# Optimization experiments

Hardware: AMD Instinct MI355X
Metric: run time of the kernel (lower is better)

## Reference

```python
import jax, jax.numpy as jnp
import numpy as np

B, H, W, L, R = 8, 32, 32, 6, 384
NH = 6                      # num_heads
NE = L * R                  # n_embd = 2304
HID = 4 * NE                # tree-MLP hidden
M = sum(4 ** i for i in range(L))  # 1365 unique tree nodes
EPS = 1e-5


def build_node_id_map(h, w, l):
    # (h,w,level) -> unique node id; level k patches are 2^k x 2^k blocks
    ids = np.zeros((h, w, l), np.int32)
    off = 0
    for k in range(l):
        ws = w >> k
        hh = (np.arange(h) >> k)[:, None]
        ww = (np.arange(w) >> k)[None, :]
        ids[:, :, k] = off + hh * ws + ww
        off += (h >> k) * ws
    assert off == M
    return ids

_IDS = jnp.asarray(build_node_id_map(H, W, L).reshape(-1))  # (H*W*L,)


def layernorm(x, w, b):
    mu = jnp.mean(x, axis=-1, keepdims=True)
    var = jnp.mean(jnp.square(x - mu), axis=-1, keepdims=True)
    return (x - mu) * jax.lax.rsqrt(var + EPS) * w + b


def setup_inputs() -> dict:
    key = jax.random.key(0)
    ks = jax.random.split(key, 12)
    s = 0.02
    return {
        "x": jax.random.normal(ks[0], (B, H, W, L, R), jnp.float32),
        "ln1_w": jnp.ones((R,), jnp.float32), "ln1_b": jnp.zeros((R,), jnp.float32),
        "ln2_w": jnp.ones((R,), jnp.float32), "ln2_b": jnp.zeros((R,), jnp.float32),
        "wq": s * jax.random.normal(ks[1], (R, R), jnp.float32), "bq": jnp.zeros((R,), jnp.float32),
        "wk": s * jax.random.normal(ks[2], (R, R), jnp.float32), "bk": jnp.zeros((R,), jnp.float32),
        "wv": s * jax.random.normal(ks[3], (R, R), jnp.float32), "bv": jnp.zeros((R,), jnp.float32),
        "wo": s * jax.random.normal(ks[4], (R, R), jnp.float32), "bo": jnp.zeros((R,), jnp.float32),
        "w1": s * jax.random.normal(ks[5], (NE, HID), jnp.float32), "b1": jnp.zeros((HID,), jnp.float32),
        "w2": s * jax.random.normal(ks[6], (HID, NE), jnp.float32), "b2": jnp.zeros((NE,), jnp.float32),
    }


def reference(x, ln1_w, ln1_b, ln2_w, ln2_b, wq, bq, wk, bk, wv, bv, wo, bo, w1, b1, w2, b2):
    dh = R // NH
    # (1) LN per node
    x_ln = layernorm(x, ln1_w, ln1_b)
    # (2) unify duplicates -> (B, M, R) via segment mean over node ids
    xf = x_ln.reshape(B, H * W * L, R)
    counts = jnp.zeros((M,), x.dtype).at[_IDS].add(1.0)
    uniq = jnp.zeros((B, M, R), x.dtype).at[:, _IDS].add(xf) / counts[None, :, None]
    # (3) multi-head self-attention over the M unique tree nodes
    q = (uniq @ wq + bq).reshape(B, M, NH, dh)
    k = (uniq @ wk + bk).reshape(B, M, NH, dh)
    v = (uniq @ wv + bv).reshape(B, M, NH, dh)
    logits = jnp.einsum("bmhd,bnhd->bhmn", q, k) * (1.0 / jnp.sqrt(jnp.asarray(dh, x.dtype)))
    attn = jax.nn.softmax(logits, axis=-1)
    o = jnp.einsum("bhmn,bnhd->bmhd", attn, v).reshape(B, M, R)
    attn_out = o @ wo + bo
    # (4) scatter back to (B,H,W,L,R)
    x_attn = attn_out[:, _IDS].reshape(B, H, W, L, R)
    # (5) residual (dropout is identity in eval)
    x_res = x + x_attn
    # (6) LN -> tree MLP over full level stack at each (h,w)
    x_ln2 = layernorm(x_res, ln2_w, ln2_b)
    flat = x_ln2.reshape(B, H, W, NE)
    h1 = jax.nn.gelu(flat @ w1 + b1)
    mlp_out = (h1 @ w2 + b2).reshape(B, H, W, L, R)
    # (7) residual
    return x_res + mlp_out
```

## Files before the change

### kernel.cpp

```cpp
#include <hip/hip_runtime.h>
#include <cstddef>

#define B_    8
#define H_    32
#define W_    32
#define L_    6
#define R_    384
#define NH_   6
#define DH_   64
#define M_    1365
#define MPAD_ 1408
#define NE_   2304
#define HID_  9216
#define NROW_ 49152
#define BMR_  10920

typedef __bf16 bf16x8 __attribute__((ext_vector_type(8)));
typedef float  f32x4  __attribute__((ext_vector_type(4)));
typedef unsigned short us;

__device__ __forceinline__ unsigned short f2b(float f){
  unsigned u = __float_as_uint(f);
  u = (u + 0x7FFFu + ((u >> 16) & 1u)) >> 16;
  return (unsigned short)u;
}

__device__ __forceinline__ void gload16(const unsigned short* g, unsigned short* l){
  __builtin_amdgcn_global_load_lds(
      (const __attribute__((address_space(1))) unsigned int*)g,
      (__attribute__((address_space(3))) unsigned int*)l,
      16, 0, 0);
}

__device__ __forceinline__ float wsum(float s){
  #pragma unroll
  for (int o = 32; o > 0; o >>= 1) s += __shfl_xor(s, o, 64);
  return s;
}

__device__ __forceinline__ float rmax16(float v){
  v = fmaxf(v, __shfl_xor(v, 1, 64));
  v = fmaxf(v, __shfl_xor(v, 2, 64));
  v = fmaxf(v, __shfl_xor(v, 4, 64));
  v = fmaxf(v, __shfl_xor(v, 8, 64));
  return v;
}
__device__ __forceinline__ float rsum16(float v){
  v += __shfl_xor(v, 1, 64);
  v += __shfl_xor(v, 2, 64);
  v += __shfl_xor(v, 4, 64);
  v += __shfl_xor(v, 8, 64);
  return v;
}

__device__ __forceinline__ float gelu_tanh(float x){
  float t = tanhf(0.7978845608028654f * (x + 0.044715f * x * x * x));
  return 0.5f * x * (1.0f + t);
}

__global__ __launch_bounds__(256) void k_ln1_scatter(
    const float* __restrict__ x, const float* __restrict__ lw,
    const float* __restrict__ lb, float* __restrict__ uniq){
  int row  = blockIdx.x * 4 + (threadIdx.x >> 6);
  int lane = threadIdx.x & 63;
  int l  = row % 6;
  int hw = (row / 6) & 1023;
  int b  = row / 6144;
  int h = hw >> 5, w = hw & 31;
  const float* xr = x + (size_t)row * R_;
  float v[6]; float s = 0.f;
  #pragma unroll
  for (int i = 0; i < 6; i++){ v[i] = xr[lane + i*64]; s += v[i]; }
  s = wsum(s);
  float mu = s * (1.f/384.f);
  float qq = 0.f;
  #pragma unroll
  for (int i = 0; i < 6; i++){ float d = v[i]-mu; qq += d*d; }
  qq = wsum(qq);
  float rs = rsqrtf(qq * (1.f/384.f) + 1e-5f);
  int off = (4096 - (4096 >> (2*l))) / 3;
  int id  = off + (h >> l) * (32 >> l) + (w >> l);
  float invc = 1.f / (float)(1 << (2*l));
  float* ur = uniq + ((size_t)b * M_ + id) * R_;
  #pragma unroll
  for (int i = 0; i < 6; i++){
    int r = lane + i*64;
    float ln = (v[i]-mu)*rs*lw[r] + lb[r];
    atomicAdd(&ur[r], ln * invc);
  }
}

__global__ void k_cvt(const float* __restrict__ src, unsigned short* __restrict__ dst, int n){
  int i = blockIdx.x * 256 + threadIdx.x;
  if (i < n) dst[i] = f2b(src[i]);
}

__global__ void k_tcvt(const float* __restrict__ src, unsigned short* __restrict__ dst,
                       int K, int N){
  __shared__ float t[32][33];
  int n0 = blockIdx.x * 32, k0 = blockIdx.y * 32;
  int tx = threadIdx.x, ty = threadIdx.y;
  #pragma unroll
  for (int i = 0; i < 4; i++)
    t[ty + i*8][tx] = src[(size_t)(k0 + ty + i*8) * N + n0 + tx];
  __syncthreads();
  #pragma unroll
  for (int i = 0; i < 4; i++)
    dst[(size_t)(n0 + ty + i*8) * K + k0 + tx] = f2b(t[tx][ty + i*8]);
}

template<int EPI>
__global__ __launch_bounds__(256) void k_gemm(
    const unsigned short* __restrict__ A,
    const unsigned short* __restrict__ Bt,
    const float* __restrict__ bias,
    void* __restrict__ Cout,
    const float* __restrict__ res,
    void* __restrict__ aux1, void* __restrict__ aux2,
    int Mtot, int N, int K){
  __shared__ unsigned short As[128*64];
  __shared__ unsigned short Bs[128*64];
  int m0 = blockIdx.x * 128, n0 = blockIdx.y * 128;
  int tid  = threadIdx.x;
  int wv   = tid >> 6, lane = tid & 63;
  int quad = lane >> 4, l16 = lane & 15;
  int wm = (wv >> 1) * 64, wn = (wv & 1) * 64;
  int lr = lane >> 3;
  int lc = (lane & 7) * 8;
  f32x4 acc[4][4];
  #pragma unroll
  for (int a = 0; a < 4; a++)
    #pragma unroll
    for (int bidx = 0; bidx < 4; bidx++) acc[a][bidx] = 0.f;

  for (int k0 = 0; k0 < K; k0 += 64){
    #pragma unroll
    for (int j = 0; j < 4; j++){
      int c = wv*4 + j;
      int rowa = c*8 + lr;
      int gm = m0 + rowa; if (gm >= Mtot) gm = Mtot - 1;
      gload16(A + (size_t)gm * K + k0 + lc, &As[c*512]);
      int gn = n0 + rowa;
      gload16(Bt + (size_t)gn * K + k0 + lc, &Bs[c*512]);
    }
    asm volatile("s_waitcnt vmcnt(0)" ::: "memory");
    __syncthreads();
    #pragma unroll
    for (int ko = 0; ko < 2; ko++){
      bf16x8 af[4], bfr[4];
      #pragma unroll
      for (int t = 0; t < 4; t++){
        af[t]  = *(const bf16x8*)(&As[(wm + t*16 + l16)*64 + ko*32 + quad*8]);
        bfr[t] = *(const bf16x8*)(&Bs[(wn + t*16 + l16)*64 + ko*32 + quad*8]);
      }
      #pragma unroll
      for (int mt = 0; mt < 4; mt++)
        #pragma unroll
        for (int nt = 0; nt < 4; nt++)
          acc[mt][nt] = __builtin_amdgcn_mfma_f32_16x16x32_bf16(
              af[mt], bfr[nt], acc[mt][nt], 0, 0, 0);
    }
    __syncthreads();
  }
  #pragma unroll
  for (int mt = 0; mt < 4; mt++){
    #pragma unroll
    for (int i = 0; i < 4; i++){
      int row = m0 + wm + mt*16 + quad*4 + i;
      if (row >= Mtot) continue;
      #pragma unroll
      for (int nt = 0; nt < 4; nt++){
        int col = n0 + wn + nt*16 + l16;
        size_t idx = (size_t)row * N + col;
        float vv = acc[mt][nt][i] + bias[col];
        if (EPI == 5){
          int bb = row / M_;
          int mm = row - bb * M_;
          if (col < 384){
            ((unsigned short*)Cout)[(size_t)row * R_ + col] = f2b(vv);
          } else if (col < 768){
            ((unsigned short*)aux1)[(size_t)row * R_ + col - 384] = f2b(vv);
          } else {
            int c2 = col - 768;
            int hh = c2 >> 6, dd = c2 & 63;
            ((unsigned short*)aux2)[(((size_t)(bb*NH_ + hh))*DH_ + dd)*MPAD_ + mm] = f2b(vv);
          }
        } else {
          ((float*)Cout)[idx] = vv;
        }
      }
    }
  }
}


__device__ __forceinline__ void stage_half(const unsigned short* __restrict__ g,
                                           unsigned short* l, int K){
  int tid = threadIdx.x;
  int w  = tid >> 6;
  int ln = tid & 63;
  int rw = ln >> 3;
  int cs = ((ln & 7) ^ rw) * 8;
  gload16(g + (size_t)(w*16 + rw)     * K + cs, l + (w*16)*64);
  gload16(g + (size_t)(w*16 + 8 + rw) * K + cs, l + (w*16 + 8)*64);
}

__device__ __forceinline__ bf16x8 ldsfrag(const unsigned short* base, int row, int ko, int quad){
  int g = ((ko << 2) + quad) ^ (row & 7);
  return *(const bf16x8*)(base + row*64 + g*8);
}

#define PH_BAR()   asm volatile("s_barrier" ::: "memory")
#define PH_LGKM0() asm volatile("s_waitcnt lgkmcnt(0)" ::: "memory")

#define APHASE(MTBASE)                                                                 \
  {                                                                                    \
    bf16x8 af0l = ldsfrag(curA, wr*128 + (MTBASE)*16   + l16, 0, quad);                \
    bf16x8 af0h = ldsfrag(curA, wr*128 + (MTBASE)*16   + l16, 1, quad);                \
    bf16x8 af1l = ldsfrag(curA, wr*128 + (MTBASE+1)*16 + l16, 0, quad);                \
    bf16x8 af1h = ldsfrag(curA, wr*128 + (MTBASE+1)*16 + l16, 1, quad);                \
    PH_BAR(); PH_LGKM0();                                                              \
    __builtin_amdgcn_s_setprio(1);                                                     \
    _Pragma("unroll")                                                                  \
    for (int nt = 0; nt < 4; nt++){                                                    \
      acc[MTBASE][nt]   = __builtin_amdgcn_mfma_f32_16x16x32_bf16(af0l, bfr[nt][0], acc[MTBASE][nt],   0,0,0); \
      acc[MTBASE][nt]   = __builtin_amdgcn_mfma_f32_16x16x32_bf16(af0h, bfr[nt][1], acc[MTBASE][nt],   0,0,0); \
      acc[MTBASE+1][nt] = __builtin_amdgcn_mfma_f32_16x16x32_bf16(af1l, bfr[nt][0], acc[MTBASE+1][nt], 0,0,0); \
      acc[MTBASE+1][nt] = __builtin_amdgcn_mfma_f32_16x16x32_bf16(af1h, bfr[nt][1], acc[MTBASE+1][nt], 0,0,0); \
    }                                                                                  \
    __builtin_amdgcn_s_setprio(0);                                                     \
  }

template<int EPI>
__global__ __launch_bounds__(512, 2) void k_gemm8(
    const unsigned short* __restrict__ A,
    const unsigned short* __restrict__ Bt,
    const float* __restrict__ bias,
    void* __restrict__ Cout,
    int Mtot, int N, int Kfull, int kLen){
  __shared__ unsigned short lds8[2][32768];

  int m0 = blockIdx.x * 256, n0 = blockIdx.y * 256;
  int k0 = blockIdx.z * kLen;
  int NT = kLen >> 6;
  const size_t KS = (size_t)Kfull;
  const us* Ab = A  + (size_t)m0 * KS + k0;
  const us* Bb = Bt + (size_t)n0 * KS + k0;
  int tid = threadIdx.x, wv = tid >> 6, lane = tid & 63;
  int quad = lane >> 4, l16 = lane & 15;
  int wr = wv >> 2, wc = wv & 3;

  f32x4 acc[8][4];
  #pragma unroll
  for (int a = 0; a < 8; a++)
    #pragma unroll
    for (int b = 0; b < 4; b++) acc[a][b] = 0.f;

  stage_half(Bb,               &lds8[0][16384],        Kfull);
  stage_half(Bb + 128*KS,      &lds8[0][16384 + 8192], Kfull);
  stage_half(Ab,               &lds8[0][0],            Kfull);
  stage_half(Ab + 128*KS,      &lds8[0][8192],         Kfull);
  if (NT > 1){
    stage_half(Bb + 64,             &lds8[1][16384],        Kfull);
    stage_half(Bb + 128*KS + 64,    &lds8[1][16384 + 8192], Kfull);
    asm volatile("s_waitcnt vmcnt(4)" ::: "memory");
  } else {
    asm volatile("s_waitcnt vmcnt(0)" ::: "memory");
  }
  PH_BAR();

  for (int t = 0; t < NT; ++t){
    us* curA = &lds8[t & 1][0];
    us* curB = curA + 16384;
    us* nxtA = &lds8[(t + 1) & 1][0];
    bool st1 = (t + 1 < NT), st2 = (t + 2 < NT);
    const us* An = Ab + (size_t)(t + 1) * 64;
    const us* Bn = Bb + (size_t)(t + 2) * 64;
    bf16x8 bfr[4][2];

    if (st1) stage_half(An, nxtA, Kfull);
    #pragma unroll
    for (int nt = 0; nt < 4; nt++){
      bfr[nt][0] = ldsfrag(curB, wc*64 + nt*16 + l16, 0, quad);
      bfr[nt][1] = ldsfrag(curB, wc*64 + nt*16 + l16, 1, quad);
    }
    APHASE(0);
    PH_BAR();

    if (st1) stage_half(An + 128*KS, nxtA + 8192, Kfull);
    APHASE(2);
    PH_BAR();

    if (st2) stage_half(Bn, curB, Kfull);
    APHASE(4);
    PH_BAR();

    if (st2) stage_half(Bn + 128*KS, curB + 8192, Kfull);
    APHASE(6);
    if (st1){
      if (st2) asm volatile("s_waitcnt vmcnt(4)" ::: "memory");
      else     asm volatile("s_waitcnt vmcnt(0)" ::: "memory");
    }
    PH_BAR();
  }

  #pragma unroll
  for (int mt = 0; mt < 8; mt++){
    #pragma unroll
    for (int i = 0; i < 4; i++){
      int row = m0 + wr*128 + mt*16 + quad*4 + i;
      #pragma unroll
      for (int nt = 0; nt < 4; nt++){
        int col = n0 + wc*64 + nt*16 + l16;
        size_t idx = (size_t)row * N + col;
        float vv = acc[mt][nt][i];
        if (EPI == 1){
          ((unsigned short*)Cout)[idx] = f2b(gelu_tanh(vv + bias[col]));
        } else {
          atomicAdd(&((float*)Cout)[idx], vv);
        }
      }
    }
  }
}

__global__ __launch_bounds__(256) void k_attn(
    const unsigned short* __restrict__ qb, const unsigned short* __restrict__ kb,
    const unsigned short* __restrict__ vtb, unsigned short* __restrict__ ob){
  __shared__ unsigned short Ks[64][64];
  __shared__ unsigned short Vt[64][64];
  __shared__ unsigned short Ps[4][16][64];
  int qt = blockIdx.x, bh = blockIdx.y;
  int b = bh / NH_, h = bh % NH_;
  int tid = threadIdx.x, wv = tid >> 6, lane = tid & 63;
  int quad = lane >> 4, l16 = lane & 15;

  int qm = qt*64 + wv*16 + l16;
  const unsigned short* qrow = qb + (size_t)(b*M_ + qm)*R_ + h*DH_;
  bf16x8 aq0 = *(const bf16x8*)(qrow + quad*8);
  bf16x8 aq1 = *(const bf16x8*)(qrow + 32 + quad*8);

  f32x4 oacc[4];
  #pragma unroll
  for (int db = 0; db < 4; db++) oacc[db] = 0.f;
  float mi[4], li[4];
  #pragma unroll
  for (int i = 0; i < 4; i++){ mi[i] = -1e30f; li[i] = 0.f; }

  for (int kt = 0; kt < 22; kt++){
    #pragma unroll
    for (int i = 0; i < 2; i++){
      int c = tid + i*256;
      int rowa = c >> 3, colc = (c & 7) * 8;
      *(uint4*)(&Ks[rowa][colc]) =
        *(const uint4*)(kb + (size_t)(b*M_ + kt*64 + rowa)*R_ + h*DH_ + colc);
      *(uint4*)(&Vt[rowa][colc]) =
        *(const uint4*)(vtb + ((size_t)bh*DH_ + rowa)*MPAD_ + kt*64 + colc);
    }
    __syncthreads();

    f32x4 s[4];
    #pragma unroll
    for (int nb = 0; nb < 4; nb++){
      s[nb] = 0.f;
      bf16x8 bk0 = *(const bf16x8*)(&Ks[nb*16 + l16][quad*8]);
      bf16x8 bk1 = *(const bf16x8*)(&Ks[nb*16 + l16][32 + quad*8]);
      s[nb] = __builtin_amdgcn_mfma_f32_16x16x32_bf16(aq0, bk0, s[nb], 0, 0, 0);
      s[nb] = __builtin_amdgcn_mfma_f32_16x16x32_bf16(aq1, bk1, s[nb], 0, 0, 0);
    }

    #pragma unroll
    for (int i = 0; i < 4; i++){
      float val[4];
      float mx = -1e30f;
      #pragma unroll
      for (int nb = 0; nb < 4; nb++){
        int gc = kt*64 + nb*16 + l16;
        val[nb] = (gc < M_) ? s[nb][i] * 0.125f : -1e30f;
        mx = fmaxf(mx, val[nb]);
      }
      mx = rmax16(mx);
      float mnew = fmaxf(mi[i], mx);
      float alpha = __expf(mi[i] - mnew);
      float rs = 0.f;
      #pragma unroll
      for (int nb = 0; nb < 4; nb++){
        float p = __expf(val[nb] - mnew);
        rs += p;
        Ps[wv][quad*4 + i][nb*16 + l16] = f2b(p);
      }
      rs = rsum16(rs);
      li[i] = li[i]*alpha + rs;
      mi[i] = mnew;
      #pragma unroll
      for (int db = 0; db < 4; db++) oacc[db][i] *= alpha;
    }

    #pragma unroll
    for (int ko = 0; ko < 2; ko++){
      bf16x8 ap = *(const bf16x8*)(&Ps[wv][l16][ko*32 + quad*8]);
      #pragma unroll
      for (int db = 0; db < 4; db++){
        bf16x8 bv = *(const bf16x8*)(&Vt[db*16 + l16][ko*32 + quad*8]);
        oacc[db] = __builtin_amdgcn_mfma_f32_16x16x32_bf16(ap, bv, oacc[db], 0, 0, 0);
      }
    }
    __syncthreads();
  }

  #pragma unroll
  for (int i = 0; i < 4; i++){
    int gm = qt*64 + wv*16 + quad*4 + i;
    if (gm < M_){
      float il = 1.f / li[i];
      #pragma unroll
      for (int db = 0; db < 4; db++)
        ob[(size_t)(b*M_ + gm)*R_ + h*DH_ + db*16 + l16] = f2b(oacc[db][i] * il);
    }
  }
}

__global__ __launch_bounds__(256) void k_scatter_ln2(
    const float* __restrict__ x, const float* __restrict__ attn,
    const float* __restrict__ lw, const float* __restrict__ lb,
    const float* __restrict__ b2,
    float* __restrict__ xres, unsigned short* __restrict__ flatb){
  int row  = blockIdx.x * 4 + (threadIdx.x >> 6);
  int lane = threadIdx.x & 63;
  int l  = row % 6;
  int hw = (row / 6) & 1023;
  int b  = row / 6144;
  int h = hw >> 5, w = hw & 31;
  int off = (4096 - (4096 >> (2*l))) / 3;
  int id  = off + (h >> l) * (32 >> l) + (w >> l);
  const float* ar = attn + ((size_t)b * M_ + id) * R_;
  const float* xr = x + (size_t)row * R_;
  float* orow = xres + (size_t)row * R_;
  float vv[6]; float s = 0.f;
  #pragma unroll
  for (int i = 0; i < 6; i++){
    int r = lane + i*64;
    float t = xr[r] + ar[r];
    vv[i] = t; s += t;
    orow[r] = t + b2[l*R_ + r];
  }
  s = wsum(s);
  float mu = s * (1.f/384.f);
  float qq = 0.f;
  #pragma unroll
  for (int i = 0; i < 6; i++){ float d = vv[i]-mu; qq += d*d; }
  qq = wsum(qq);
  float rs = rsqrtf(qq * (1.f/384.f) + 1e-5f);
  unsigned short* fr = flatb + (size_t)row * R_;
  #pragma unroll
  for (int i = 0; i < 6; i++){
    int r = lane + i*64;
    fr[r] = f2b((vv[i]-mu)*rs*lw[r] + lb[r]);
  }
}

extern "C" void kernel_launch(void* const* d_in, const int* in_sizes, int n_in,
                              void* d_out, int out_size, void* d_ws, size_t ws_size,
                              hipStream_t stream){
  const float* x    = (const float*)d_in[0];
  const float* ln1w = (const float*)d_in[1];
  const float* ln1b = (const float*)d_in[2];
  const float* ln2w = (const float*)d_in[3];
  const float* ln2b = (const float*)d_in[4];
  const float* wq   = (const float*)d_in[5];
  const float* bq   = (const float*)d_in[6];
  const float* wk   = (const float*)d_in[7];
  const float* bk   = (const float*)d_in[8];
  const float* wvv  = (const float*)d_in[9];
  const float* bv   = (const float*)d_in[10];
  const float* wo   = (const float*)d_in[11];
  const float* bo   = (const float*)d_in[12];
  const float* w1   = (const float*)d_in[13];
  const float* b1   = (const float*)d_in[14];
  const float* w2   = (const float*)d_in[15];
  const float* b2   = (const float*)d_in[16];
  float* out = (float*)d_out;

  char* ws = (char*)d_ws;
  unsigned short* h1b = (unsigned short*)ws;
  unsigned short* qb  = (unsigned short*)ws;
  unsigned short* kb  = qb + (size_t)BMR_ * R_;
  unsigned short* vtb = kb + (size_t)BMR_ * R_;
  unsigned short* ob  = vtb + (size_t)B_ * NH_ * DH_ * MPAD_;
  float* attn_o = (float*)(ob + (size_t)BMR_ * R_);
  size_t regA = ((size_t)8192 * HID_ * 2 + 255) & ~(size_t)255;
  char* p = ws + regA;
  float* uniqf = (float*)p;                   p += (size_t)BMR_ * R_ * 4;
  unsigned short* uniqb = (unsigned short*)p; p += (size_t)BMR_ * R_ * 2;
  unsigned short* wqkvt = (unsigned short*)p; p += (size_t)3 * R_ * R_ * 2;
  unsigned short* wot = (unsigned short*)p;   p += (size_t)R_ * R_ * 2;
  unsigned short* w1t = (unsigned short*)p;   p += (size_t)NE_ * HID_ * 2;
  unsigned short* w2t = (unsigned short*)p;   p += (size_t)NE_ * HID_ * 2;
  unsigned short* flatb = (unsigned short*)p; p += (size_t)NROW_ * R_ * 2;
  float* bqkv = (float*)p;                    p += (size_t)3 * R_ * 4;

  hipMemsetAsync(uniqf, 0, (size_t)BMR_ * R_ * 4, stream);
  hipMemsetAsync(vtb, 0, (size_t)B_ * NH_ * DH_ * MPAD_ * 2, stream);
  hipMemcpyAsync(bqkv,        bq, R_*4, hipMemcpyDeviceToDevice, stream);
  hipMemcpyAsync(bqkv + R_,   bk, R_*4, hipMemcpyDeviceToDevice, stream);
  hipMemcpyAsync(bqkv + 2*R_, bv, R_*4, hipMemcpyDeviceToDevice, stream);

  k_ln1_scatter<<<NROW_/4, 256, 0, stream>>>(x, ln1w, ln1b, uniqf);
  k_cvt<<<(BMR_*R_ + 255)/256, 256, 0, stream>>>(uniqf, uniqb, BMR_*R_);

  dim3 tb(32, 8);
  k_tcvt<<<dim3(R_/32, R_/32), tb, 0, stream>>>(wq, wqkvt, R_, R_);
  k_tcvt<<<dim3(R_/32, R_/32), tb, 0, stream>>>(wk, wqkvt + (size_t)R_*R_, R_, R_);
  k_tcvt<<<dim3(R_/32, R_/32), tb, 0, stream>>>(wvv, wqkvt + (size_t)2*R_*R_, R_, R_);
  k_tcvt<<<dim3(R_/32, R_/32), tb, 0, stream>>>(wo, wot, R_, R_);
  k_tcvt<<<dim3(HID_/32, NE_/32), tb, 0, stream>>>(w1, w1t, NE_, HID_);
  k_tcvt<<<dim3(NE_/32, HID_/32), tb, 0, stream>>>(w2, w2t, HID_, NE_);

  k_gemm<5><<<dim3(86, 9), 256, 0, stream>>>(uniqb, wqkvt, bqkv, qb, nullptr,
                                             kb, vtb, BMR_, 3*R_, R_);

  k_attn<<<dim3(22, 48), 256, 0, stream>>>(qb, kb, vtb, ob);

  k_gemm<0><<<dim3(86, 3), 256, 0, stream>>>(ob, wot, bo, attn_o, nullptr,
                                             nullptr, nullptr, BMR_, R_, R_);

  k_scatter_ln2<<<NROW_/4, 256, 0, stream>>>(x, attn_o, ln2w, ln2b, b2, out, flatb);

  k_gemm8<1><<<dim3(32, 36), 512, 0, stream>>>(flatb, w1t, b1, h1b,
                                               8192, HID_, NE_, NE_);
  k_gemm8<3><<<dim3(32, 9, 2), 512, 0, stream>>>(h1b, w2t, nullptr, out,
                                                 8192, NE_, HID_, HID_/2);
}
```

Baseline: 1.503 ms.

## Cut GEMM main-loop barriers to two per tile and use sigmoid-form GELU

The bf16 GEMM main loop drops from four barriers per K-tile to two. Both A-half stages are issued up front, A fragments are prefetched into registers ahead of their MFMA clusters, and sched_barrier fences keep the compiler from reordering across the barriers. The aim is to cut barrier stalls and overlap LDS reads with MFMA work. The GELU epilogue now uses the algebraically equivalent x*sigmoid(2u) form with __expf in place of tanhf, which is cheaper but slightly less accurate, and prefetching the fragments raises register pressure.

```diff
diff --git a/kernel.cpp b/kernel.cpp
--- a/kernel.cpp
+++ b/kernel.cpp
@@ -53,9 +53,9 @@
   return v;
 }
 
-__device__ __forceinline__ float gelu_tanh(float x){
-  float t = tanhf(0.7978845608028654f * (x + 0.044715f * x * x * x));
-  return 0.5f * x * (1.0f + t);
+__device__ __forceinline__ float gelu_fast(float x){
+  float t = fmaf(0.07135482f * x, x * x, 1.5957691216f * x);
+  return x / (1.0f + __expf(-t));
 }
 
 __global__ __launch_bounds__(256) void k_ln1_scatter(
@@ -210,23 +210,16 @@
   return *(const bf16x8*)(base + row*64 + g*8);
 }
 
-#define PH_BAR()   asm volatile("s_barrier" ::: "memory")
-#define PH_LGKM0() asm volatile("s_waitcnt lgkmcnt(0)" ::: "memory")
-
-#define APHASE(MTBASE)                                                                 \
+#define SB0()      __builtin_amdgcn_sched_barrier(0)
+#define CLUSTER(I0, I1, F0, F1)                                                        \
   {                                                                                    \
-    bf16x8 af0l = ldsfrag(curA, wr*128 + (MTBASE)*16   + l16, 0, quad);                \
-    bf16x8 af0h = ldsfrag(curA, wr*128 + (MTBASE)*16   + l16, 1, quad);                \
-    bf16x8 af1l = ldsfrag(curA, wr*128 + (MTBASE+1)*16 + l16, 0, quad);                \
-    bf16x8 af1h = ldsfrag(curA, wr*128 + (MTBASE+1)*16 + l16, 1, quad);                \
-    PH_BAR(); PH_LGKM0();                                                              \
     __builtin_amdgcn_s_setprio(1);                                                     \
     _Pragma("unroll")                                                                  \
     for (int nt = 0; nt < 4; nt++){                                                    \
-      acc[MTBASE][nt]   = __builtin_amdgcn_mfma_f32_16x16x32_bf16(af0l, bfr[nt][0], acc[MTBASE][nt],   0,0,0); \
-      acc[MTBASE][nt]   = __builtin_amdgcn_mfma_f32_16x16x32_bf16(af0h, bfr[nt][1], acc[MTBASE][nt],   0,0,0); \
-      acc[MTBASE+1][nt] = __builtin_amdgcn_mfma_f32_16x16x32_bf16(af1l, bfr[nt][0], acc[MTBASE+1][nt], 0,0,0); \
-      acc[MTBASE+1][nt] = __builtin_amdgcn_mfma_f32_16x16x32_bf16(af1h, bfr[nt][1], acc[MTBASE+1][nt], 0,0,0); \
+      acc[I0][nt] = __builtin_amdgcn_mfma_f32_16x16x32_bf16(F0[0], bfr[nt][0], acc[I0][nt], 0,0,0); \
+      acc[I0][nt] = __builtin_amdgcn_mfma_f32_16x16x32_bf16(F0[1], bfr[nt][1], acc[I0][nt], 0,0,0); \
+      acc[I1][nt] = __builtin_amdgcn_mfma_f32_16x16x32_bf16(F1[0], bfr[nt][0], acc[I1][nt], 0,0,0); \
+      acc[I1][nt] = __builtin_amdgcn_mfma_f32_16x16x32_bf16(F1[1], bfr[nt][1], acc[I1][nt], 0,0,0); \
     }                                                                                  \
     __builtin_amdgcn_s_setprio(0);                                                     \
   }
@@ -267,7 +260,8 @@
   } else {
     asm volatile("s_waitcnt vmcnt(0)" ::: "memory");
   }
-  PH_BAR();
+  asm volatile("s_barrier" ::: "memory");
+  SB0();
 
   for (int t = 0; t < NT; ++t){
     us* curA = &lds8[t & 1][0];
@@ -276,32 +270,53 @@
     bool st1 = (t + 1 < NT), st2 = (t + 2 < NT);
     const us* An = Ab + (size_t)(t + 1) * 64;
     const us* Bn = Bb + (size_t)(t + 2) * 64;
-    bf16x8 bfr[4][2];
-
-    if (st1) stage_half(An, nxtA, Kfull);
+
+    bf16x8 bfr[4][2], aA[4][2], aB[2][2], aC[2][2];
     #pragma unroll
     for (int nt = 0; nt < 4; nt++){
       bfr[nt][0] = ldsfrag(curB, wc*64 + nt*16 + l16, 0, quad);
       bfr[nt][1] = ldsfrag(curB, wc*64 + nt*16 + l16, 1, quad);
     }
-    APHASE(0);
-    PH_BAR();
-
-    if (st1) stage_half(An + 128*KS, nxtA + 8192, Kfull);
-    APHASE(2);
-    PH_BAR();
-
-    if (st2) stage_half(Bn, curB, Kfull);
-    APHASE(4);
-    PH_BAR();
-
-    if (st2) stage_half(Bn + 128*KS, curB + 8192, Kfull);
-    APHASE(6);
+    #pragma unroll
+    for (int mt = 0; mt < 4; mt++){
+      aA[mt][0] = ldsfrag(curA, wr*128 + mt*16 + l16, 0, quad);
+      aA[mt][1] = ldsfrag(curA, wr*128 + mt*16 + l16, 1, quad);
+    }
+    if (st1){
+      stage_half(An,          nxtA,        Kfull);
+      stage_half(An + 128*KS, nxtA + 8192, Kfull);
+    }
+
+    CLUSTER(0, 1, aA[0], aA[1]);
+    #pragma unroll
+    for (int mt = 0; mt < 2; mt++){
+      aB[mt][0] = ldsfrag(curA, wr*128 + (4+mt)*16 + l16, 0, quad);
+      aB[mt][1] = ldsfrag(curA, wr*128 + (4+mt)*16 + l16, 1, quad);
+    }
+    CLUSTER(2, 3, aA[2], aA[3]);
+
+    SB0();
+    __builtin_amdgcn_s_barrier();
+    SB0();
+    if (st2){
+      stage_half(Bn,          curB,        Kfull);
+      stage_half(Bn + 128*KS, curB + 8192, Kfull);
+    }
+    #pragma unroll
+    for (int mt = 0; mt < 2; mt++){
+      aC[mt][0] = ldsfrag(curA, wr*128 + (6+mt)*16 + l16, 0, quad);
+      aC[mt][1] = ldsfrag(curA, wr*128 + (6+mt)*16 + l16, 1, quad);
+    }
+    CLUSTER(4, 5, aB[0], aB[1]);
+    CLUSTER(6, 7, aC[0], aC[1]);
+
     if (st1){
       if (st2) asm volatile("s_waitcnt vmcnt(4)" ::: "memory");
       else     asm volatile("s_waitcnt vmcnt(0)" ::: "memory");
     }
-    PH_BAR();
+    SB0();
+    __builtin_amdgcn_s_barrier();
+    SB0();
   }
 
   #pragma unroll
@@ -315,7 +330,7 @@
         size_t idx = (size_t)row * N + col;
         float vv = acc[mt][nt][i];
         if (EPI == 1){
-          ((unsigned short*)Cout)[idx] = f2b(gelu_tanh(vv + bias[col]));
+          ((unsigned short*)Cout)[idx] = f2b(gelu_fast(vv + bias[col]));
         } else {
           atomicAdd(&((float*)Cout)[idx], vv);
         }
```

New measurement: 1.415 ms. 5.9% less time.

## Unroll GEMM K-loop by two with sched barriers and a sigmoid-form GELU

Applied to the files above, without the earlier changes.

The bf16 MFMA GEMM main loop is unrolled by two so LDS buffer indices become compile-time constants. Each phase now issues its global-to-LDS stage after the A-fragment LDS reads, and sched_barrier fences pin that ordering. MFMAs within a phase are regrouped so consecutive instructions hit independent accumulators. Separately, the tanh GELU in the first MLP epilogue is rewritten as the equivalent x*sigmoid(2z) using a fast exp, to cut epilogue cost. The unrolled loop assumes an even number of K tiles per block; an odd count would run one extra tile past the end.

```diff
diff --git a/kernel.cpp b/kernel.cpp
--- a/kernel.cpp
+++ b/kernel.cpp
@@ -53,9 +53,9 @@
   return v;
 }
 
-__device__ __forceinline__ float gelu_tanh(float x){
-  float t = tanhf(0.7978845608028654f * (x + 0.044715f * x * x * x));
-  return 0.5f * x * (1.0f + t);
+__device__ __forceinline__ float gelu_fast(float x){
+  float t = fmaf(0.07135482f * x, x * x, 1.5957691216f * x);
+  return x / (1.0f + __expf(-t));
 }
 
 __global__ __launch_bounds__(256) void k_ln1_scatter(
@@ -210,26 +210,60 @@
   return *(const bf16x8*)(base + row*64 + g*8);
 }
 
-#define PH_BAR()   asm volatile("s_barrier" ::: "memory")
-#define PH_LGKM0() asm volatile("s_waitcnt lgkmcnt(0)" ::: "memory")
-
-#define APHASE(MTBASE)                                                                 \
-  {                                                                                    \
-    bf16x8 af0l = ldsfrag(curA, wr*128 + (MTBASE)*16   + l16, 0, quad);                \
-    bf16x8 af0h = ldsfrag(curA, wr*128 + (MTBASE)*16   + l16, 1, quad);                \
-    bf16x8 af1l = ldsfrag(curA, wr*128 + (MTBASE+1)*16 + l16, 0, quad);                \
-    bf16x8 af1h = ldsfrag(curA, wr*128 + (MTBASE+1)*16 + l16, 1, quad);                \
-    PH_BAR(); PH_LGKM0();                                                              \
-    __builtin_amdgcn_s_setprio(1);                                                     \
-    _Pragma("unroll")                                                                  \
-    for (int nt = 0; nt < 4; nt++){                                                    \
-      acc[MTBASE][nt]   = __builtin_amdgcn_mfma_f32_16x16x32_bf16(af0l, bfr[nt][0], acc[MTBASE][nt],   0,0,0); \
-      acc[MTBASE][nt]   = __builtin_amdgcn_mfma_f32_16x16x32_bf16(af0h, bfr[nt][1], acc[MTBASE][nt],   0,0,0); \
-      acc[MTBASE+1][nt] = __builtin_amdgcn_mfma_f32_16x16x32_bf16(af1l, bfr[nt][0], acc[MTBASE+1][nt], 0,0,0); \
-      acc[MTBASE+1][nt] = __builtin_amdgcn_mfma_f32_16x16x32_bf16(af1h, bfr[nt][1], acc[MTBASE+1][nt], 0,0,0); \
-    }                                                                                  \
-    __builtin_amdgcn_s_setprio(0);                                                     \
-  }
+#define SB0()  __builtin_amdgcn_sched_barrier(0)
+#define MFMA16(A8, B8, C4) __builtin_amdgcn_mfma_f32_16x16x32_bf16(A8, B8, C4, 0, 0, 0)
+
+#define PHASE(P, STAGE_STMT, TAIL_STMT)                                          \
+  { bf16x8 aL0 = ldsfrag(curA, wr*128 + (2*(P))*16   + l16, 0, quad);            \
+    bf16x8 aH0 = ldsfrag(curA, wr*128 + (2*(P))*16   + l16, 1, quad);            \
+    bf16x8 aL1 = ldsfrag(curA, wr*128 + (2*(P)+1)*16 + l16, 0, quad);            \
+    bf16x8 aH1 = ldsfrag(curA, wr*128 + (2*(P)+1)*16 + l16, 1, quad);            \
+    STAGE_STMT;                                                                  \
+    SB0();                                                                       \
+    __builtin_amdgcn_s_barrier();                                                \
+    asm volatile("s_waitcnt lgkmcnt(0)" ::: "memory");                           \
+    SB0();                                                                       \
+    __builtin_amdgcn_s_setprio(1);                                               \
+    _Pragma("unroll")                                                            \
+    for (int nt = 0; nt < 4; nt++)                                               \
+      acc[2*(P)][nt]   = MFMA16(aL0, bfr[nt][0], acc[2*(P)][nt]);                \
+    _Pragma("unroll")                                                            \
+    for (int nt = 0; nt < 4; nt++)                                               \
+      acc[2*(P)+1][nt] = MFMA16(aL1, bfr[nt][0], acc[2*(P)+1][nt]);              \
+    _Pragma("unroll")                                                            \
+    for (int nt = 0; nt < 4; nt++)                                               \
+      acc[2*(P)][nt]   = MFMA16(aH0, bfr[nt][1], acc[2*(P)][nt]);                \
+    _Pragma("unroll")                                                            \
+    for (int nt = 0; nt < 4; nt++)                                               \
+      acc[2*(P)+1][nt] = MFMA16(aH1, bfr[nt][1], acc[2*(P)+1][nt]);              \
+    __builtin_amdgcn_s_setprio(0);                                               \
+    TAIL_STMT;                                                                   \
+    SB0();                                                                       \
+    __builtin_amdgcn_s_barrier();                                                \
+    SB0(); }
+
+#define KTILE(CURBUF)                                                            \
+  { us* curA = &lds8[CURBUF][0];                                                 \
+    us* curB = curA + 16384;                                                     \
+    us* nxtA = &lds8[(CURBUF) ^ 1][0];                                           \
+    bool st1 = (t + 1 < NT), st2 = (t + 2 < NT);                                 \
+    const us* An = Ab + (size_t)(t + 1) * 64;                                    \
+    const us* Bn = Bb + (size_t)(t + 2) * 64;                                    \
+    bf16x8 bfr[4][2];                                                            \
+    _Pragma("unroll")                                                            \
+    for (int nt = 0; nt < 4; nt++){                                              \
+      bfr[nt][0] = ldsfrag(curB, wc*64 + nt*16 + l16, 0, quad);                  \
+      bfr[nt][1] = ldsfrag(curB, wc*64 + nt*16 + l16, 1, quad);                  \
+    }                                                                            \
+    PHASE(0, { if (st1) stage_half(An,          nxtA,        Kfull); }, {});     \
+    PHASE(1, { if (st1) stage_half(An + 128*KS, nxtA + 8192, Kfull); }, {});     \
+    PHASE(2, { if (st2) stage_half(Bn,          curB,        Kfull); }, {});     \
+    PHASE(3, { if (st2) stage_half(Bn + 128*KS, curB + 8192, Kfull); },          \
+             { if (st1){                                                         \
+                 if (st2) asm volatile("s_waitcnt vmcnt(4)" ::: "memory");       \
+                 else     asm volatile("s_waitcnt vmcnt(0)" ::: "memory");       \
+               } });                                                             \
+    ++t; }
 
 template<int EPI>
 __global__ __launch_bounds__(512, 2) void k_gemm8(
@@ -267,41 +301,13 @@
   } else {
     asm volatile("s_waitcnt vmcnt(0)" ::: "memory");
   }
-  PH_BAR();
-
-  for (int t = 0; t < NT; ++t){
-    us* curA = &lds8[t & 1][0];
-    us* curB = curA + 16384;
-    us* nxtA = &lds8[(t + 1) & 1][0];
-    bool st1 = (t + 1 < NT), st2 = (t + 2 < NT);
-    const us* An = Ab + (size_t)(t + 1) * 64;
-    const us* Bn = Bb + (size_t)(t + 2) * 64;
-    bf16x8 bfr[4][2];
-
-    if (st1) stage_half(An, nxtA, Kfull);
-    #pragma unroll
-    for (int nt = 0; nt < 4; nt++){
-      bfr[nt][0] = ldsfrag(curB, wc*64 + nt*16 + l16, 0, quad);
-      bfr[nt][1] = ldsfrag(curB, wc*64 + nt*16 + l16, 1, quad);
-    }
-    APHASE(0);
-    PH_BAR();
-
-    if (st1) stage_half(An + 128*KS, nxtA + 8192, Kfull);
-    APHASE(2);
-    PH_BAR();
-
-    if (st2) stage_half(Bn, curB, Kfull);
-    APHASE(4);
-    PH_BAR();
-
-    if (st2) stage_half(Bn + 128*KS, curB + 8192, Kfull);
-    APHASE(6);
-    if (st1){
-      if (st2) asm volatile("s_waitcnt vmcnt(4)" ::: "memory");
-      else     asm volatile("s_waitcnt vmcnt(0)" ::: "memory");
-    }
-    PH_BAR();
+  __builtin_amdgcn_s_barrier();
+  SB0();
+
+  int t = 0;
+  while (t < NT){
+    KTILE(0);
+    KTILE(1);
   }
 
   #pragma unroll
@@ -315,7 +321,7 @@
         size_t idx = (size_t)row * N + col;
         float vv = acc[mt][nt][i];
         if (EPI == 1){
-          ((unsigned short*)Cout)[idx] = f2b(gelu_tanh(vv + bias[col]));
+          ((unsigned short*)Cout)[idx] = f2b(gelu_fast(vv + bias[col]));
         } else {
           atomicAdd(&((float*)Cout)[idx], vv);
         }
```

Result: faster. 1.453 ms (-3.3%).
